# Kernel optimization log

Hardware: AMD Instinct MI355X
Metric: run time of the kernel (lower is better)

Reference implementation:

```python
import jax, jax.numpy as jnp
import numpy as np


def _deform_unfold(feat, offset):
    """Deformable 3x3 unfold with bilinear sampling, zero padding outside.
    feat: [B,C,H,W], offset: [B,2K,H,W] (y,x per point). Returns [B,C,K,H,W]."""
    B, C, H, W = feat.shape
    K = offset.shape[1] // 2
    off = offset.reshape(B, K, 2, H, W)
    # 3x3 kernel grid, dilation 1, padding 1 -> relative taps in {-1,0,1}
    ky = (jnp.arange(K) // 3 - 1).astype(feat.dtype)
    kx = (jnp.arange(K) % 3 - 1).astype(feat.dtype)
    hh = jnp.arange(H, dtype=feat.dtype)
    ww = jnp.arange(W, dtype=feat.dtype)
    py = hh[None, None, :, None] + ky[None, :, None, None] + off[:, :, 0]  # [B,K,H,W]
    px = ww[None, None, None, :] + kx[None, :, None, None] + off[:, :, 1]  # [B,K,H,W]
    y0 = jnp.floor(py)
    x0 = jnp.floor(px)
    fy = py - y0  # frac weights
    fx = px - x0
    y0i = y0.astype(jnp.int32)
    x0i = x0.astype(jnp.int32)

    def gather(yi, xi):
        valid = ((yi >= 0) & (yi < H) & (xi >= 0) & (xi < W)).astype(feat.dtype)
        yc = jnp.clip(yi, 0, H - 1)
        xc = jnp.clip(xi, 0, W - 1)
        v = jax.vmap(lambda f, yy, xx: f[:, yy, xx])(feat, yc, xc)  # [B,C,K,H,W]
        return v * valid[:, None]

    w00 = ((1 - fy) * (1 - fx))[:, None]
    w01 = ((1 - fy) * fx)[:, None]
    w10 = (fy * (1 - fx))[:, None]
    w11 = (fy * fx)[:, None]
    return (gather(y0i, x0i) * w00 + gather(y0i, x0i + 1) * w01 +
            gather(y0i + 1, x0i) * w10 + gather(y0i + 1, x0i + 1) * w11)


def setup_inputs() -> dict:
    key = jax.random.key(0)
    ks = jax.random.split(key, 8)
    B, C, H, W = 4, 256, 64, 64
    Ci, P = 128, 9
    x = jax.random.normal(ks[0], (B, C, H, W), jnp.float32)
    offset = jax.random.normal(ks[1], (B, 2 * P, H, W), jnp.float32)
    std = 0.01  # normal_init(std=0.01)
    Wq = jax.random.normal(ks[2], (Ci, C), jnp.float32) * std
    Wk = jax.random.normal(ks[3], (Ci, C), jnp.float32) * std
    Wv = jax.random.normal(ks[4], (Ci, C), jnp.float32) * std
    Wo = jax.random.normal(ks[5], (Ci,), jnp.float32) * std
    bq = jnp.zeros((Ci,), jnp.float32)
    bk = jnp.zeros((Ci,), jnp.float32)
    bv = jnp.zeros((Ci,), jnp.float32)
    bo = jnp.zeros((1,), jnp.float32)
    return {"x": x, "offset": offset, "Wq": Wq, "bq": bq, "Wk": Wk, "bk": bk,
            "Wv": Wv, "bv": bv, "Wo": Wo, "bo": bo}


def reference(x, offset, Wq, bq, Wk, bk, Wv, bv, Wo, bo):
    # 1x1 conv projections
    q = jnp.einsum('bchw,oc->bohw', x, Wq) + bq[None, :, None, None]
    k = jnp.einsum('bchw,oc->bohw', x, Wk) + bk[None, :, None, None]
    v = jnp.einsum('bchw,oc->bohw', x, Wv) + bv[None, :, None, None]
    qu = _deform_unfold(q, offset)  # [B,Ci,K,H,W]
    ku = _deform_unfold(k, offset)  # [B,Ci,K,H,W]
    vu = _deform_unfold(v, offset)  # [B,Ci,K,H,W]
    # per-pixel KxK attention: query [K,Ci] @ key [Ci,K]
    scores = jnp.einsum('bcihw,bcjhw->bijhw', qu, ku)  # [B,K,K,H,W]
    attn = jax.nn.softmax(scores, axis=2)
    # attn [K,K] @ value [K,Ci]
    out_v = jnp.einsum('bijhw,bcjhw->bcihw', attn, vu)  # [B,Ci,K,H,W]
    # conv_out: 1x1 conv Ci->1 over the value, then sigmoid -> [B,K,H,W]
    out = jnp.einsum('bcihw,c->bihw', out_v, Wo) + bo[0]
    return jax.nn.sigmoid(out)
```

## Files before the change

### kernel.cpp

```cpp
#include <hip/hip_runtime.h>

typedef unsigned short u16;
typedef unsigned int u32;

#define B_   4
#define C_   256
#define CI_  128
#define H_   64
#define W_   64
#define NPB_ 4096
#define NP_  16384
#define K_   9
#define MROWS_ 272

typedef __attribute__((ext_vector_type(8))) __bf16 bf16x8_t;
typedef __attribute__((ext_vector_type(4))) float f32x4_t;
typedef __attribute__((ext_vector_type(2))) float f32x2_t;
typedef __attribute__((ext_vector_type(4))) u32 u32x4;

#define GLD(dst, p, immstr) \
    asm volatile("global_load_dwordx4 %0, %1, off offset:" immstr \
                 : "=v"(dst) : "v"(p))

__device__ __forceinline__ float bf2f_lo(u32 w) {
    union { u32 i; float f; } x; x.i = w << 16; return x.f;
}
__device__ __forceinline__ float bf2f_hi(u32 w) {
    union { u32 i; float f; } x; x.i = w & 0xffff0000u; return x.f;
}
__device__ __forceinline__ u16 f2bf(float f) {
    union { float f; u32 i; } x; x.f = f;
    u32 lsb = (x.i >> 16) & 1u;
    return (u16)((x.i + 0x7fffu + lsb) >> 16);
}
__device__ __forceinline__ void acc8p(f32x2_t* f, u32x4 v, f32x2_t w2) {
    f32x2_t p;
    p.x = bf2f_lo(v[0]); p.y = bf2f_hi(v[0]); f[0] += w2 * p;
    p.x = bf2f_lo(v[1]); p.y = bf2f_hi(v[1]); f[1] += w2 * p;
    p.x = bf2f_lo(v[2]); p.y = bf2f_hi(v[2]); f[2] += w2 * p;
    p.x = bf2f_lo(v[3]); p.y = bf2f_hi(v[3]); f[3] += w2 * p;
}

__global__ void k0b_prep(const float* __restrict__ Wq, const float* __restrict__ bq,
                         const float* __restrict__ Wk, const float* __restrict__ bk,
                         const float* __restrict__ Wv, const float* __restrict__ bv,
                         const float* __restrict__ Wo,
                         u16* __restrict__ Wt, float* __restrict__ bias) {
    const int o = blockIdx.x;
    const int c = threadIdx.x;
    u16 val;
    if (o < 128) {
        val = f2bf(Wq[o * C_ + c]);
        if (c == 0) bias[o] = bq[o];
    } else if (o < 256) {
        val = f2bf(Wk[(o - 128) * C_ + c]);
        if (c == 0) bias[o] = bk[o - 128];
    } else if (o == 256) {
        float s = 0.f;
        #pragma unroll 8
        for (int oo = 0; oo < CI_; ++oo)
            s += Wo[oo] * Wv[oo * C_ + c];
        val = f2bf(s);
        if (c == 0) {
            float ts = 0.f;
            #pragma unroll 8
            for (int oo = 0; oo < CI_; ++oo) ts += Wo[oo] * bv[oo];
            bias[256] = ts;
        }
    } else {
        val = 0;
        if (c == 0) bias[o] = 0.f;
    }
    const int mt = o >> 4, l16 = o & 15;
    const int kk = c >> 5, g = (c >> 3) & 3, e = c & 7;
    Wt[(size_t)((mt * 8 + kk) * 64 + g * 16 + l16) * 8 + e] = val;
}

__global__ __launch_bounds__(512) void k1_proj(
    const float* __restrict__ x, const u16* __restrict__ Wt,
    const float* __restrict__ bias,
    u16* __restrict__ qk, float* __restrict__ vs) {
    __shared__ u16 xs[16][272];
    const int t = threadIdx.x;
    const int l = t & 63;
    const int w = t >> 6;
    const int lane16 = l & 15;
    const int g = l >> 4;
    const int p0 = blockIdx.x * 16;
    const int b = p0 >> 12;
    const int pin = p0 & 4095;

    const int mts[3] = {2 * w, 2 * w + 1, 16};

    u32x4 afr[8][3];
    #pragma unroll
    for (int n = 0; n < 3; ++n) {
        const u16* pA = Wt + ((size_t)(mts[n] * 8) * 64 + l) * 8;
        const u16* pB = pA + 4 * 64 * 8;
        GLD(afr[0][n], pA, "0");    GLD(afr[1][n], pA, "1024");
        GLD(afr[2][n], pA, "2048"); GLD(afr[3][n], pA, "3072");
        GLD(afr[4][n], pB, "0");    GLD(afr[5][n], pB, "1024");
        GLD(afr[6][n], pB, "2048"); GLD(afr[7][n], pB, "3072");
    }

    {
        const int spx = t & 15, cg = t >> 4;
        const float* src = x + (size_t)(b * C_ + cg * 8) * NPB_ + pin + spx;
        float v[8];
        #pragma unroll
        for (int i = 0; i < 8; ++i) v[i] = src[(size_t)i * NPB_];
        uint4 pk;
        pk.x = (u32)f2bf(v[0]) | ((u32)f2bf(v[1]) << 16);
        pk.y = (u32)f2bf(v[2]) | ((u32)f2bf(v[3]) << 16);
        pk.z = (u32)f2bf(v[4]) | ((u32)f2bf(v[5]) << 16);
        pk.w = (u32)f2bf(v[6]) | ((u32)f2bf(v[7]) << 16);
        *reinterpret_cast<uint4*>(&xs[spx][cg * 8]) = pk;
    }
    __syncthreads();
    asm volatile("s_waitcnt vmcnt(0)" ::: "memory");
    __builtin_amdgcn_sched_barrier(0);

    f32x4_t acc[3];
    #pragma unroll
    for (int n = 0; n < 3; ++n)
        #pragma unroll
        for (int r = 0; r < 4; ++r)
            acc[n][r] = bias[mts[n] * 16 + g * 4 + r];

    #pragma unroll
    for (int kk = 0; kk < 8; ++kk) {
        const bf16x8_t bv = *reinterpret_cast<const bf16x8_t*>(&xs[lane16][kk * 32 + g * 8]);
        #pragma unroll
        for (int n = 0; n < 3; ++n) {
            const bf16x8_t av = __builtin_bit_cast(bf16x8_t, afr[kk][n]);
            acc[n] = __builtin_amdgcn_mfma_f32_16x16x32_bf16(av, bv, acc[n], 0, 0, 0);
        }
    }

    const int px = p0 + lane16;
    u16* qrow = qk + (size_t)px * C_;
    #pragma unroll
    for (int n = 0; n < 2; ++n) {
        const int mt = mts[n];
        u32* dst = reinterpret_cast<u32*>(qrow + mt * 16 + g * 4);
        dst[0] = (u32)f2bf(acc[n][0]) | ((u32)f2bf(acc[n][1]) << 16);
        dst[1] = (u32)f2bf(acc[n][2]) | ((u32)f2bf(acc[n][3]) << 16);
    }
    if (w == 0 && g == 0) vs[px] = acc[2][0];
}

__global__ __launch_bounds__(256) void k2_attn(
    const float* __restrict__ off, const u16* __restrict__ qk,
    const float* __restrict__ vs, const float* __restrict__ bo,
    float* __restrict__ out) {
    const int t = threadIdx.x;
    const int l = t & 63;
    const int bid = blockIdx.x;
    const int swz = (bid & 7) * ((int)gridDim.x >> 3) + (bid >> 3);
    const int pixel = swz * 4 + (t >> 6);
    const int b = pixel >> 12;
    const int rem = pixel & 4095;
    const int y = rem >> 6, xx = rem & 63;
    const int l16 = l & 15;
    const int tap = (l16 < K_) ? l16 : (K_ - 1);
    const int g = l >> 4;

    const float* offb = off + ((size_t)b * (2 * K_) + 2 * tap) * NPB_ + rem;
    const float oy = offb[0];
    const float ox = offb[NPB_];
    const float py = (float)(y + tap / 3 - 1) + oy;
    const float px = (float)(xx + tap % 3 - 1) + ox;
    const float fy0 = floorf(py), fx0 = floorf(px);
    const float fy = py - fy0, fx = px - fx0;
    const int y0 = (int)fy0, x0 = (int)fx0;

    const u16* qkb = qk + ((size_t)(b << 12)) * C_ + g * 8;
    const float* vsm = vs + (b << 12);

    float wgt[4];
    int ppc[4];
    const u16* bp[4];
    #pragma unroll
    for (int c = 0; c < 4; ++c) {
        const int dy = c >> 1, dx = c & 1;
        const int yi = y0 + dy, xi = x0 + dx;
        const float wv = (dy ? fy : 1.f - fy) * (dx ? fx : 1.f - fx);
        const int ok = (yi >= 0) & (yi < H_) & (xi >= 0) & (xi < W_);
        const int yc = min(max(yi, 0), H_ - 1);
        const int xc = min(max(xi, 0), W_ - 1);
        ppc[c] = yc * W_ + xc;
        wgt[c] = ok ? wv : 0.f;
        bp[c] = qkb + (size_t)ppc[c] * C_;
    }

    u32x4 gq[4][4], gk[4][4];
    #pragma unroll
    for (int c = 0; c < 4; ++c) {
        const u16* p = bp[c];
        GLD(gq[c][0], p, "0");   GLD(gq[c][1], p, "64");
        GLD(gq[c][2], p, "128"); GLD(gq[c][3], p, "192");
        GLD(gk[c][0], p, "256"); GLD(gk[c][1], p, "320");
        GLD(gk[c][2], p, "384"); GLD(gk[c][3], p, "448");
    }
    float vsc[4];
    #pragma unroll
    for (int c = 0; c < 4; ++c) vsc[c] = vsm[ppc[c]];
    asm volatile("s_waitcnt vmcnt(0)" ::: "memory");
    __builtin_amdgcn_sched_barrier(0);

    const float vsu_t = wgt[0] * vsc[0] + wgt[1] * vsc[1] +
                        wgt[2] * vsc[2] + wgt[3] * vsc[3];

    f32x2_t fq[16], fk[16];
    #pragma unroll
    for (int e = 0; e < 16; ++e) { fq[e] = (f32x2_t){0.f, 0.f}; fk[e] = (f32x2_t){0.f, 0.f}; }
    #pragma unroll
    for (int s = 0; s < 4; ++s) {
        #pragma unroll
        for (int c = 0; c < 4; ++c) {
            const f32x2_t w2 = {wgt[c], wgt[c]};
            acc8p(&fq[s * 4], gq[c][s], w2);
            acc8p(&fk[s * 4], gk[c][s], w2);
        }
    }

    f32x4_t acc = {0.f, 0.f, 0.f, 0.f};
    #pragma unroll
    for (int s = 0; s < 4; ++s) {
        bf16x8_t av, bv;
        #pragma unroll
        for (int e = 0; e < 4; ++e) {
            av[2 * e]     = (__bf16)fk[s * 4 + e].x;
            av[2 * e + 1] = (__bf16)fk[s * 4 + e].y;
            bv[2 * e]     = (__bf16)fq[s * 4 + e].x;
            bv[2 * e + 1] = (__bf16)fq[s * 4 + e].y;
        }
        acc = __builtin_amdgcn_mfma_f32_16x16x32_bf16(av, bv, acc, 0, 0, 0);
    }

    float mx = -1e30f;
    #pragma unroll
    for (int r = 0; r < 4; ++r) {
        const int j = g * 4 + r;
        if (j < K_) mx = fmaxf(mx, acc[r]);
    }
    mx = fmaxf(mx, __shfl_xor(mx, 16, 64));
    mx = fmaxf(mx, __shfl_xor(mx, 32, 64));

    float vj[4];
    #pragma unroll
    for (int r = 0; r < 4; ++r) vj[r] = __shfl(vsu_t, g * 4 + r, 64);

    float den = 0.f, num = 0.f;
    #pragma unroll
    for (int r = 0; r < 4; ++r) {
        const int j = g * 4 + r;
        if (j < K_) {
            const float e = __expf(acc[r] - mx);
            den += e;
            num += e * vj[r];
        }
    }
    den += __shfl_xor(den, 16, 64); den += __shfl_xor(den, 32, 64);
    num += __shfl_xor(num, 16, 64); num += __shfl_xor(num, 32, 64);

    if (l < K_) {
        const float z = num / den + bo[0];
        out[(size_t)b * K_ * NPB_ + (size_t)l * NPB_ + rem] = 1.f / (1.f + __expf(-z));
    }
}

extern "C" void kernel_launch(void* const* d_in, const int* in_sizes, int n_in,
                              void* d_out, int out_size, void* d_ws, size_t ws_size,
                              hipStream_t stream) {
    const float* x   = (const float*)d_in[0];
    const float* off = (const float*)d_in[1];
    const float* Wq  = (const float*)d_in[2];
    const float* bq  = (const float*)d_in[3];
    const float* Wk  = (const float*)d_in[4];
    const float* bk  = (const float*)d_in[5];
    const float* Wv  = (const float*)d_in[6];
    const float* bv  = (const float*)d_in[7];
    const float* Wo  = (const float*)d_in[8];
    const float* bo  = (const float*)d_in[9];
    float* out = (float*)d_out;

    char* ws = (char*)d_ws;
    u16*   qkbuf = (u16*)(ws + 4096);
    float* vsmap = (float*)(ws + 4096 + 8388608);
    u16*   Wt    = (u16*)(ws + 4096 + 8388608 + 65536);
    float* bias  = (float*)(ws + 4096 + 8388608 + 65536 + 139264);

    k0b_prep<<<MROWS_, 256, 0, stream>>>(Wq, bq, Wk, bk, Wv, bv, Wo, Wt, bias);
    k1_proj<<<NP_ / 16, 512, 0, stream>>>(x, Wt, bias, qkbuf, vsmap);
    k2_attn<<<NP_ / 4, 256, 0, stream>>>(off, qkbuf, vsmap, bo, out);
}
```

Baseline: 75.44 us.

## Split each pixel's channel reduction across four waves with LDS reduce

The attention kernel now assigns one pixel per block and splits the 128-channel q·k reduction across four waves, each loading and MFMA-ing a 32-channel slice. Partial score tiles are summed through shared memory, and wave 0 finishes the softmax and output. This cuts per-thread registers and serial load/MFMA chains to raise memory-level parallelism. In exchange it launches four times as many blocks, adds a __syncthreads and LDS traffic, and leaves three waves idle after the reduction.

```diff
diff --git a/kernel.cpp b/kernel.cpp
--- a/kernel.cpp
+++ b/kernel.cpp
@@ -153,11 +153,12 @@
     const float* __restrict__ off, const u16* __restrict__ qk,
     const float* __restrict__ vs, const float* __restrict__ bo,
     float* __restrict__ out) {
+    __shared__ f32x4_t red[3][64];
     const int t = threadIdx.x;
     const int l = t & 63;
+    const int w = t >> 6;
     const int bid = blockIdx.x;
-    const int swz = (bid & 7) * ((int)gridDim.x >> 3) + (bid >> 3);
-    const int pixel = swz * 4 + (t >> 6);
+    const int pixel = (bid & 7) * (NP_ / 8) + (bid >> 3);
     const int b = pixel >> 12;
     const int rem = pixel & 4095;
     const int y = rem >> 6, xx = rem & 63;
@@ -174,7 +175,7 @@
     const float fy = py - fy0, fx = px - fx0;
     const int y0 = (int)fy0, x0 = (int)fx0;
 
-    const u16* qkb = qk + ((size_t)(b << 12)) * C_ + g * 8;
+    const u16* qkbase = qk + ((size_t)(b << 12)) * C_ + w * 32 + g * 8;
     const float* vsm = vs + (b << 12);
 
     float wgt[4];
@@ -190,53 +191,54 @@
         const int xc = min(max(xi, 0), W_ - 1);
         ppc[c] = yc * W_ + xc;
         wgt[c] = ok ? wv : 0.f;
-        bp[c] = qkb + (size_t)ppc[c] * C_;
-    }
-
-    u32x4 gq[4][4], gk[4][4];
+        bp[c] = qkbase + (size_t)ppc[c] * C_;
+    }
+
+    u32x4 gq[4], gk[4];
     #pragma unroll
     for (int c = 0; c < 4; ++c) {
-        const u16* p = bp[c];
-        GLD(gq[c][0], p, "0");   GLD(gq[c][1], p, "64");
-        GLD(gq[c][2], p, "128"); GLD(gq[c][3], p, "192");
-        GLD(gk[c][0], p, "256"); GLD(gk[c][1], p, "320");
-        GLD(gk[c][2], p, "384"); GLD(gk[c][3], p, "448");
+        GLD(gq[c], bp[c], "0");
+        GLD(gk[c], bp[c], "256");
     }
     float vsc[4];
-    #pragma unroll
-    for (int c = 0; c < 4; ++c) vsc[c] = vsm[ppc[c]];
+    if (w == 0) {
+        #pragma unroll
+        for (int c = 0; c < 4; ++c) vsc[c] = vsm[ppc[c]];
+    }
     asm volatile("s_waitcnt vmcnt(0)" ::: "memory");
     __builtin_amdgcn_sched_barrier(0);
 
+    f32x2_t fq[4], fk[4];
+    #pragma unroll
+    for (int e = 0; e < 4; ++e) { fq[e] = (f32x2_t){0.f, 0.f}; fk[e] = (f32x2_t){0.f, 0.f}; }
+    #pragma unroll
+    for (int c = 0; c < 4; ++c) {
+        const f32x2_t w2 = {wgt[c], wgt[c]};
+        acc8p(fq, gq[c], w2);
+        acc8p(fk, gk[c], w2);
+    }
+
+    bf16x8_t av, bv;
+    #pragma unroll
+    for (int e = 0; e < 4; ++e) {
+        av[2 * e]     = (__bf16)fk[e].x;
+        av[2 * e + 1] = (__bf16)fk[e].y;
+        bv[2 * e]     = (__bf16)fq[e].x;
+        bv[2 * e + 1] = (__bf16)fq[e].y;
+    }
+    f32x4_t acc = {0.f, 0.f, 0.f, 0.f};
+    acc = __builtin_amdgcn_mfma_f32_16x16x32_bf16(av, bv, acc, 0, 0, 0);
+
+    if (w > 0) red[w - 1][l] = acc;
+    __syncthreads();
+    if (w != 0) return;
+
+    acc += red[0][l];
+    acc += red[1][l];
+    acc += red[2][l];
+
     const float vsu_t = wgt[0] * vsc[0] + wgt[1] * vsc[1] +
                         wgt[2] * vsc[2] + wgt[3] * vsc[3];
-
-    f32x2_t fq[16], fk[16];
-    #pragma unroll
-    for (int e = 0; e < 16; ++e) { fq[e] = (f32x2_t){0.f, 0.f}; fk[e] = (f32x2_t){0.f, 0.f}; }
-    #pragma unroll
-    for (int s = 0; s < 4; ++s) {
-        #pragma unroll
-        for (int c = 0; c < 4; ++c) {
-            const f32x2_t w2 = {wgt[c], wgt[c]};
-            acc8p(&fq[s * 4], gq[c][s], w2);
-            acc8p(&fk[s * 4], gk[c][s], w2);
-        }
-    }
-
-    f32x4_t acc = {0.f, 0.f, 0.f, 0.f};
-    #pragma unroll
-    for (int s = 0; s < 4; ++s) {
-        bf16x8_t av, bv;
-        #pragma unroll
-        for (int e = 0; e < 4; ++e) {
-            av[2 * e]     = (__bf16)fk[s * 4 + e].x;
-            av[2 * e + 1] = (__bf16)fk[s * 4 + e].y;
-            bv[2 * e]     = (__bf16)fq[s * 4 + e].x;
-            bv[2 * e + 1] = (__bf16)fq[s * 4 + e].y;
-        }
-        acc = __builtin_amdgcn_mfma_f32_16x16x32_bf16(av, bv, acc, 0, 0, 0);
-    }
 
     float mx = -1e30f;
     #pragma unroll
@@ -293,5 +295,5 @@
 
     k0b_prep<<<MROWS_, 256, 0, stream>>>(Wq, bq, Wk, bk, Wv, bv, Wo, Wt, bias);
     k1_proj<<<NP_ / 16, 512, 0, stream>>>(x, Wt, bias, qkbuf, vsmap);
-    k2_attn<<<NP_ / 4, 256, 0, stream>>>(off, qkbuf, vsmap, bo, out);
-}
+    k2_attn<<<NP_, 256, 0, stream>>>(off, qkbuf, vsmap, bo, out);
+}
```

Measured after the change: 77.11 us. +2.2%, slower.
